# Optimization experiments

Hardware: AMD Instinct MI355X
Metric: run time of the kernel (lower is better)

Reference implementation:

```python
import jax, jax.numpy as jnp
import numpy as np

_BYPASS_THR = 0.99          # assumed v16._BYPASS_THR
_EML_CLAMP = 10000.0        # eml_clamp passed to __init__
COMPLEX = jnp.complex64     # v16.DTYPE


def eml_exact(l, r):
    # EML 'exact' combine: exp(log(l) * log(r)) in the complex domain.
    # This continuous relaxation reproduces mul/pow/add-like behaviour used
    return jnp.exp(jnp.log(l) * jnp.log(r))


def setup_inputs() -> dict:
    key = jax.random.key(0)
    k1, k2, k3, k4 = jax.random.split(key, 4)
    S, depth, B = 16, 5, 131072
    n_leaves = 2 ** depth          # 32
    n_internal = n_leaves - 1      # 31
    x = jax.random.normal(k1, (B,), dtype=jnp.float32)
    y = jax.random.normal(k2, (B,), dtype=jnp.float32)
    # 'uniform' init strategy: leaf ~ N(0,1)*scale, gate ~ N(0,1)*scale + 4
    leaf_logits = jax.random.normal(k3, (S, n_leaves, 3), dtype=jnp.float32)
    blend_logits = jax.random.normal(k4, (S, n_internal, 2), dtype=jnp.float32) + 4.0
    return {"x": x, "y": y, "leaf_logits": leaf_logits, "blend_logits": blend_logits}


def reference(x, y, leaf_logits, blend_logits):
    tau_leaf = 1.0
    tau_gate = 1.0
    C = _EML_CLAMP

    leaf_probs = jax.nn.softmax(leaf_logits / tau_leaf, axis=2)     # (S, L, 3)
    weights = leaf_probs.astype(COMPLEX)

    xc = x.astype(COMPLEX)
    yc = y.astype(COMPLEX)
    ones = jnp.ones_like(xc)
    candidates = jnp.stack([ones, xc, yc], axis=1)                  # (B, 3)

    # current_level: (S, B, n_leaves) complex
    current = jnp.einsum('bc,slc->sbl', candidates, weights)

    gate_levels = []
    eml_outputs = []
    node_idx = 0
    while current.shape[2] > 1:
        n_pairs = current.shape[2] // 2
        left = current[:, :, 0::2]                                  # (S,B,P)
        right = current[:, :, 1::2]
        s = jax.nn.sigmoid(blend_logits[:, node_idx:node_idx + n_pairs] / tau_gate)  # (S,P,2)
        gate_levels.append(s)
        s_left = s[:, :, 0][:, None, :]                             # (S,1,P)
        s_right = s[:, :, 1][:, None, :]
        byp_l = s_left > _BYPASS_THR
        byp_r = s_right > _BYPASS_THR
        oml = 1.0 - s_left
        omr = 1.0 - s_right
        lr = jnp.where(byp_l, 1.0, s_left + oml * left.real)
        li = jnp.where(byp_l, 0.0, oml * left.imag)
        rr = jnp.where(byp_r, 1.0, s_right + omr * right.real)
        ri = jnp.where(byp_r, 0.0, omr * right.imag)
        out = eml_exact(jax.lax.complex(lr, li), jax.lax.complex(rr, ri))
        re = jnp.clip(jnp.nan_to_num(out.real, nan=0.0, posinf=C, neginf=-C), -C, C)
        im = jnp.clip(jnp.nan_to_num(out.imag, nan=0.0, posinf=C, neginf=-C), -C, C)
        current = jax.lax.complex(re, im)
        eml_outputs.append(current)
        node_idx += n_pairs

    gate_probs = jnp.concatenate(gate_levels, axis=1)               # (S, n_internal, 2)
    pred = current[:, :, 0]                                         # (S, B) complex
    return (pred, leaf_probs, gate_probs, *eml_outputs)
```

## Files before the change

### kernel.cpp

```cpp
#include <hip/hip_runtime.h>
#include <math.h>

#define C_CLAMP 10000.0f
#define BYP 0.99f
#define LN2F 0.6931471805599453f

constexpr int NL  = 32;
constexpr int NI  = 31;
constexpr int NG  = 15;
constexpr int BLK = 256;

typedef float f4 __attribute__((ext_vector_type(4)));
typedef float f2 __attribute__((ext_vector_type(2)));

template<bool HASIM>
__device__ __forceinline__ void eml_op(float lre, float lim, float rre, float rim,
                                       float& ore, float& oim) {
    bool ok = fminf(lre, rre) > 0.0f;
    if constexpr (HASIM)
        ok = ok & (fmaxf(fabsf(lim), fabsf(rim)) == 0.0f);

    float t = __log2f(lre) * __log2f(rre);
    float e = __builtin_amdgcn_exp2f(t * LN2F);
    ore = fminf(e, C_CLAMP);
    oim = 0.0f;

    if (__any(!ok)) {
        float a = 0.5f * logf(fmaf(lre, lre, lim * lim));
        float b = atan2f(lim, lre);
        float c = 0.5f * logf(fmaf(rre, rre, rim * rim));
        float d = atan2f(rim, rre);
        float tt = a * c - b * d;
        float th = a * d + b * c;
        float ex = expf(tt);
        float re_ = ex * cosf(th);
        float im_ = ex * sinf(th);
        re_ = __builtin_isnan(re_) ? 0.0f : re_;
        im_ = __builtin_isnan(im_) ? 0.0f : im_;
        re_ = fminf(fmaxf(re_, -C_CLAMP), C_CLAMP);
        im_ = fminf(fmaxf(im_, -C_CLAMP), C_CLAMP);
        if (!ok) { ore = re_; oim = im_; }
    }
}

template<int NP>
__device__ __forceinline__ void do_level(const f4* g4b, int node0,
                                         const float* ire, const float* iim,
                                         float* ore, float* oim) {
#pragma unroll
    for (int p = 0; p < NP; ++p) {
        f4 gg = g4b[node0 - 16 + p];
        float lre = fmaf(gg.y, ire[2 * p],     gg.x);
        float rre = fmaf(gg.w, ire[2 * p + 1], gg.z);
        float lim = gg.y * iim[2 * p];
        float rim = gg.w * iim[2 * p + 1];
        eml_op<true>(lre, lim, rre, rim, ore[p], oim[p]);
    }
}

template<bool PAIRS, int NP>
__device__ __forceinline__ void store_lvl(float* __restrict__ dst, long long sb,
                                          const float* re, const float* im) {
    if constexpr (PAIRS) {
        float* p = dst + sb * (2 * NP);
        if constexpr (NP >= 2) {
#pragma unroll
            for (int q = 0; q < NP; q += 2)
                *reinterpret_cast<f4*>(p + 2 * q) = f4{ re[q], im[q], re[q + 1], im[q + 1] };
        } else {
            *reinterpret_cast<f2*>(p) = f2{ re[0], im[0] };
        }
    } else {
        float* p = dst + sb * NP;
        if constexpr (NP >= 4) {
#pragma unroll
            for (int q = 0; q < NP; q += 4)
                *reinterpret_cast<f4*>(p + q) = f4{ re[q], re[q + 1], re[q + 2], re[q + 3] };
        } else if constexpr (NP == 2) {
            *reinterpret_cast<f2*>(p) = f2{ re[0], re[1] };
        } else {
            p[0] = re[0];
        }
    }
}

template<bool PAIRS>
__global__ __launch_bounds__(BLK, 6) void eml_tree_kernel(
    const float* __restrict__ x, const float* __restrict__ y,
    const float* __restrict__ leaf_logits, const float* __restrict__ blend_logits,
    float* __restrict__ o_pred, float* __restrict__ o_leaf, float* __restrict__ o_gate,
    float* __restrict__ o_l1, float* __restrict__ o_l2, float* __restrict__ o_l3,
    float* __restrict__ o_l4, float* __restrict__ o_l5,
    int B, int blocksPerS)
{
    __shared__ f4    eff4[NL];
    __shared__ f4    g4b[NG];
    __shared__ float graw[NI * 2];
    __shared__ float st1[16][BLK + 1];
    __shared__ float st2[8][BLK + 1];

    const int bid   = blockIdx.x;
    const int s     = bid / blocksPerS;
    const int chunk = bid - s * blocksPerS;
    const int tid   = threadIdx.x;

    if (tid < NL) {
        const float* p = leaf_logits + (s * NL + tid) * 3;
        float a0 = p[0], a1 = p[1], a2 = p[2];
        float m  = fmaxf(a0, fmaxf(a1, a2));
        float e0 = expf(a0 - m), e1 = expf(a1 - m), e2 = expf(a2 - m);
        float inv = 1.0f / (e0 + e1 + e2);
        float w0 = e0 * inv, w1 = e1 * inv, w2 = e2 * inv;

        float sg = 1.0f / (1.0f + expf(-blend_logits[s * NI * 2 + tid]));
        graw[tid] = sg;
        if (sg > BYP) {
            eff4[tid] = f4{ 1.0f, 0.0f, 0.0f, 0.0f };
        } else {
            float om = 1.0f - sg;
            eff4[tid] = f4{ fmaf(om, w0, sg), om * w1, om * w2, 0.0f };
        }
        if (chunk == 0) {
            float* q = o_leaf + s * NL * 3 + tid * 3;
            q[0] = w0; q[1] = w1; q[2] = w2;
        }
    } else if (tid >= 64 && tid < 64 + NG) {
        int i = tid - 64;
        const float* p = blend_logits + s * NI * 2 + (16 + i) * 2;
        float sl = 1.0f / (1.0f + expf(-p[0]));
        float sr = 1.0f / (1.0f + expf(-p[1]));
        graw[(16 + i) * 2]     = sl;
        graw[(16 + i) * 2 + 1] = sr;
        bool bl = sl > BYP, br = sr > BYP;
        g4b[i] = f4{ bl ? 1.0f : sl, bl ? 0.0f : (1.0f - sl),
                     br ? 1.0f : sr, br ? 0.0f : (1.0f - sr) };
    }
    __syncthreads();

    if (chunk == 0 && tid >= 128 && tid < 128 + NI * 2)
        o_gate[s * NI * 2 + (tid - 128)] = graw[tid - 128];

    const int b = chunk * BLK + tid;
    const bool active = b < B;
    const float xv = active ? x[b] : 0.0f;
    const float yv = active ? y[b] : 0.0f;
    const long long sb = (long long)s * B + b;

    if (active) {
        float r2[8], i2[8];
        float b1r[4], b1i[4];
#pragma unroll
        for (int q = 0; q < 8; ++q) {
            const int h0 = (q & 1) * 2;
#pragma unroll
            for (int h = 0; h < 2; ++h) {
                const int p = 2 * q + h;
                f4 ea = eff4[2 * p];
                f4 eb = eff4[2 * p + 1];
                float lre = fmaf(ea.z, yv, fmaf(ea.y, xv, ea.x));
                float rre = fmaf(eb.z, yv, fmaf(eb.y, xv, eb.x));
                eml_op<false>(lre, 0.0f, rre, 0.0f, b1r[h0 + h], b1i[h0 + h]);
                if constexpr (!PAIRS) st1[p][tid] = b1r[h0 + h];
            }
            {
                f4 gg = g4b[q];
                float lre = fmaf(gg.y, b1r[h0],     gg.x);
                float rre = fmaf(gg.w, b1r[h0 + 1], gg.z);
                float lim = gg.y * b1i[h0];
                float rim = gg.w * b1i[h0 + 1];
                eml_op<true>(lre, lim, rre, rim, r2[q], i2[q]);
                if constexpr (!PAIRS) st2[q][tid] = r2[q];
            }
            if (PAIRS && (q & 1)) {
                float* pp = o_l1 + sb * 32 + (q - 1) * 4;
                *reinterpret_cast<f4*>(pp)     = f4{ b1r[0], b1i[0], b1r[1], b1i[1] };
                *reinterpret_cast<f4*>(pp + 4) = f4{ b1r[2], b1i[2], b1r[3], b1i[3] };
            }
        }
        if constexpr (PAIRS) store_lvl<PAIRS, 8>(o_l2, sb, r2, i2);

        float r3[4], i3[4];
        do_level<4>(g4b, 24, r2, i2, r3, i3);
        store_lvl<PAIRS, 4>(o_l3, sb, r3, i3);

        float r4[2], i4[2];
        do_level<2>(g4b, 28, r3, i3, r4, i4);
        store_lvl<PAIRS, 2>(o_l4, sb, r4, i4);

        float r5[1], i5[1];
        do_level<1>(g4b, 30, r4, i4, r5, i5);
        store_lvl<PAIRS, 1>(o_l5, sb, r5, i5);
        store_lvl<PAIRS, 1>(o_pred, sb, r5, i5);
    }

    if constexpr (!PAIRS) {
        __syncthreads();
        const long long b0 = (long long)s * B + (long long)chunk * BLK;
        float* dst1 = o_l1 + b0 * 16;
#pragma unroll
        for (int k = 0; k < 4; ++k) {
            int m  = tid + BLK * k;
            int bl = m >> 2, e0 = (m & 3) << 2;
            if (chunk * BLK + bl < B) {
                f4 v = { st1[e0][bl], st1[e0 + 1][bl], st1[e0 + 2][bl], st1[e0 + 3][bl] };
                *reinterpret_cast<f4*>(dst1 + 4 * (long long)m) = v;
            }
        }
        float* dst2 = o_l2 + b0 * 8;
#pragma unroll
        for (int k = 0; k < 2; ++k) {
            int m  = tid + BLK * k;
            int bl = m >> 1, e0 = (m & 1) << 2;
            if (chunk * BLK + bl < B) {
                f4 v = { st2[e0][bl], st2[e0 + 1][bl], st2[e0 + 2][bl], st2[e0 + 3][bl] };
                *reinterpret_cast<f4*>(dst2 + 4 * (long long)m) = v;
            }
        }
    }
}

extern "C" void kernel_launch(void* const* d_in, const int* in_sizes, int n_in,
                              void* d_out, int out_size, void* d_ws, size_t ws_size,
                              hipStream_t stream) {
    const float* x     = (const float*)d_in[0];
    const float* y     = (const float*)d_in[1];
    const float* leaf  = (const float*)d_in[2];
    const float* blend = (const float*)d_in[3];

    const int B = in_sizes[0];
    const int S = in_sizes[2] / (NL * 3);

    float* out = (float*)d_out;
    const long long SB = (long long)S * B;
    const long long size_pairs = SB * 64 + (long long)S * (NL * 3 + NI * 2);

    const int blocksPerS = (B + BLK - 1) / BLK;
    dim3 grid(S * blocksPerS), block(BLK);

    if ((long long)out_size >= size_pairs) {
        float* o_pred = out;
        float* o_leaf = o_pred + SB * 2;
        float* o_gate = o_leaf + (long long)S * NL * 3;
        float* o_l1   = o_gate + (long long)S * NI * 2;
        float* o_l2   = o_l1 + SB * 32;
        float* o_l3   = o_l2 + SB * 16;
        float* o_l4   = o_l3 + SB * 8;
        float* o_l5   = o_l4 + SB * 4;
        hipLaunchKernelGGL((eml_tree_kernel<true>), grid, block, 0, stream,
                           x, y, leaf, blend,
                           o_pred, o_leaf, o_gate, o_l1, o_l2, o_l3, o_l4, o_l5,
                           B, blocksPerS);
    } else {
        float* o_pred = out;
        float* o_leaf = o_pred + SB;
        float* o_gate = o_leaf + (long long)S * NL * 3;
        float* o_l1   = o_gate + (long long)S * NI * 2;
        float* o_l2   = o_l1 + SB * 16;
        float* o_l3   = o_l2 + SB * 8;
        float* o_l4   = o_l3 + SB * 4;
        float* o_l5   = o_l4 + SB * 2;
        hipLaunchKernelGGL((eml_tree_kernel<false>), grid, block, 0, stream,
                           x, y, leaf, blend,
                           o_pred, o_leaf, o_gate, o_l1, o_l2, o_l3, o_l4, o_l5,
                           B, blocksPerS);
    }
}
```

Baseline: 47.15 us.

## Use persistent-style grid with blocks looping over batch chunks per sample

The grid shrinks from one block per 256-element chunk to about 1024 blocks total, and each block strides over several chunks of the same sample. The per-sample setup (leaf softmax, gate sigmoids into shared memory) is then amortized across many chunks instead of being redone per block. Launch bounds drop from 6 to 4 waves per SIMD, which gives the compiler more registers but lowers occupancy. The non-pairs path adds an extra barrier per iteration to protect the staging buffers.

```diff
diff --git a/kernel.cpp b/kernel.cpp
--- a/kernel.cpp
+++ b/kernel.cpp
@@ -85,13 +85,13 @@
 }
 
 template<bool PAIRS>
-__global__ __launch_bounds__(BLK, 6) void eml_tree_kernel(
+__global__ __launch_bounds__(BLK, 4) void eml_tree_kernel(
     const float* __restrict__ x, const float* __restrict__ y,
     const float* __restrict__ leaf_logits, const float* __restrict__ blend_logits,
     float* __restrict__ o_pred, float* __restrict__ o_leaf, float* __restrict__ o_gate,
     float* __restrict__ o_l1, float* __restrict__ o_l2, float* __restrict__ o_l3,
     float* __restrict__ o_l4, float* __restrict__ o_l5,
-    int B, int blocksPerS)
+    int B, int blocksPerS, int kPerS)
 {
     __shared__ f4    eff4[NL];
     __shared__ f4    g4b[NG];
@@ -99,10 +99,9 @@
     __shared__ float st1[16][BLK + 1];
     __shared__ float st2[8][BLK + 1];
 
-    const int bid   = blockIdx.x;
-    const int s     = bid / blocksPerS;
-    const int chunk = bid - s * blocksPerS;
-    const int tid   = threadIdx.x;
+    const int s   = blockIdx.x / kPerS;
+    const int j   = blockIdx.x - s * kPerS;
+    const int tid = threadIdx.x;
 
     if (tid < NL) {
         const float* p = leaf_logits + (s * NL + tid) * 3;
@@ -120,7 +119,7 @@
             float om = 1.0f - sg;
             eff4[tid] = f4{ fmaf(om, w0, sg), om * w1, om * w2, 0.0f };
         }
-        if (chunk == 0) {
+        if (j == 0) {
             float* q = o_leaf + s * NL * 3 + tid * 3;
             q[0] = w0; q[1] = w1; q[2] = w2;
         }
@@ -137,84 +136,89 @@
     }
     __syncthreads();
 
-    if (chunk == 0 && tid >= 128 && tid < 128 + NI * 2)
+    if (j == 0 && tid >= 128 && tid < 128 + NI * 2)
         o_gate[s * NI * 2 + (tid - 128)] = graw[tid - 128];
 
-    const int b = chunk * BLK + tid;
-    const bool active = b < B;
-    const float xv = active ? x[b] : 0.0f;
-    const float yv = active ? y[b] : 0.0f;
-    const long long sb = (long long)s * B + b;
-
-    if (active) {
-        float r2[8], i2[8];
-        float b1r[4], b1i[4];
-#pragma unroll
-        for (int q = 0; q < 8; ++q) {
-            const int h0 = (q & 1) * 2;
-#pragma unroll
-            for (int h = 0; h < 2; ++h) {
-                const int p = 2 * q + h;
-                f4 ea = eff4[2 * p];
-                f4 eb = eff4[2 * p + 1];
-                float lre = fmaf(ea.z, yv, fmaf(ea.y, xv, ea.x));
-                float rre = fmaf(eb.z, yv, fmaf(eb.y, xv, eb.x));
-                eml_op<false>(lre, 0.0f, rre, 0.0f, b1r[h0 + h], b1i[h0 + h]);
-                if constexpr (!PAIRS) st1[p][tid] = b1r[h0 + h];
+    const long long sBase = (long long)s * B;
+
+    for (int chunk = j; chunk < blocksPerS; chunk += kPerS) {
+        const int b = chunk * BLK + tid;
+        const bool active = b < B;
+        const float xv = active ? x[b] : 0.0f;
+        const float yv = active ? y[b] : 0.0f;
+        const long long sb = sBase + b;
+
+        if (active) {
+            float r2[8], i2[8];
+            float b1r[4], b1i[4];
+#pragma unroll
+            for (int q = 0; q < 8; ++q) {
+                const int h0 = (q & 1) * 2;
+#pragma unroll
+                for (int h = 0; h < 2; ++h) {
+                    const int p = 2 * q + h;
+                    f4 ea = eff4[2 * p];
+                    f4 eb = eff4[2 * p + 1];
+                    float lre = fmaf(ea.z, yv, fmaf(ea.y, xv, ea.x));
+                    float rre = fmaf(eb.z, yv, fmaf(eb.y, xv, eb.x));
+                    eml_op<false>(lre, 0.0f, rre, 0.0f, b1r[h0 + h], b1i[h0 + h]);
+                    if constexpr (!PAIRS) st1[p][tid] = b1r[h0 + h];
+                }
+                {
+                    f4 gg = g4b[q];
+                    float lre = fmaf(gg.y, b1r[h0],     gg.x);
+                    float rre = fmaf(gg.w, b1r[h0 + 1], gg.z);
+                    float lim = gg.y * b1i[h0];
+                    float rim = gg.w * b1i[h0 + 1];
+                    eml_op<true>(lre, lim, rre, rim, r2[q], i2[q]);
+                    if constexpr (!PAIRS) st2[q][tid] = r2[q];
+                }
+                if (PAIRS && (q & 1)) {
+                    float* pp = o_l1 + sb * 32 + (q - 1) * 4;
+                    *reinterpret_cast<f4*>(pp)     = f4{ b1r[0], b1i[0], b1r[1], b1i[1] };
+                    *reinterpret_cast<f4*>(pp + 4) = f4{ b1r[2], b1i[2], b1r[3], b1i[3] };
+                }
             }
-            {
-                f4 gg = g4b[q];
-                float lre = fmaf(gg.y, b1r[h0],     gg.x);
-                float rre = fmaf(gg.w, b1r[h0 + 1], gg.z);
-                float lim = gg.y * b1i[h0];
-                float rim = gg.w * b1i[h0 + 1];
-                eml_op<true>(lre, lim, rre, rim, r2[q], i2[q]);
-                if constexpr (!PAIRS) st2[q][tid] = r2[q];
+            if constexpr (PAIRS) store_lvl<PAIRS, 8>(o_l2, sb, r2, i2);
+
+            float r3[4], i3[4];
+            do_level<4>(g4b, 24, r2, i2, r3, i3);
+            store_lvl<PAIRS, 4>(o_l3, sb, r3, i3);
+
+            float r4[2], i4[2];
+            do_level<2>(g4b, 28, r3, i3, r4, i4);
+            store_lvl<PAIRS, 2>(o_l4, sb, r4, i4);
+
+            float r5[1], i5[1];
+            do_level<1>(g4b, 30, r4, i4, r5, i5);
+            store_lvl<PAIRS, 1>(o_l5, sb, r5, i5);
+            store_lvl<PAIRS, 1>(o_pred, sb, r5, i5);
+        }
+
+        if constexpr (!PAIRS) {
+            __syncthreads();
+            const long long b0 = sBase + (long long)chunk * BLK;
+            float* dst1 = o_l1 + b0 * 16;
+#pragma unroll
+            for (int k = 0; k < 4; ++k) {
+                int m  = tid + BLK * k;
+                int bl = m >> 2, e0 = (m & 3) << 2;
+                if (chunk * BLK + bl < B) {
+                    f4 v = { st1[e0][bl], st1[e0 + 1][bl], st1[e0 + 2][bl], st1[e0 + 3][bl] };
+                    *reinterpret_cast<f4*>(dst1 + 4 * (long long)m) = v;
+                }
             }
-            if (PAIRS && (q & 1)) {
-                float* pp = o_l1 + sb * 32 + (q - 1) * 4;
-                *reinterpret_cast<f4*>(pp)     = f4{ b1r[0], b1i[0], b1r[1], b1i[1] };
-                *reinterpret_cast<f4*>(pp + 4) = f4{ b1r[2], b1i[2], b1r[3], b1i[3] };
+            float* dst2 = o_l2 + b0 * 8;
+#pragma unroll
+            for (int k = 0; k < 2; ++k) {
+                int m  = tid + BLK * k;
+                int bl = m >> 1, e0 = (m & 1) << 2;
+                if (chunk * BLK + bl < B) {
+                    f4 v = { st2[e0][bl], st2[e0 + 1][bl], st2[e0 + 2][bl], st2[e0 + 3][bl] };
+                    *reinterpret_cast<f4*>(dst2 + 4 * (long long)m) = v;
+                }
             }
-        }
-        if constexpr (PAIRS) store_lvl<PAIRS, 8>(o_l2, sb, r2, i2);
-
-        float r3[4], i3[4];
-        do_level<4>(g4b, 24, r2, i2, r3, i3);
-        store_lvl<PAIRS, 4>(o_l3, sb, r3, i3);
-
-        float r4[2], i4[2];
-        do_level<2>(g4b, 28, r3, i3, r4, i4);
-        store_lvl<PAIRS, 2>(o_l4, sb, r4, i4);
-
-        float r5[1], i5[1];
-        do_level<1>(g4b, 30, r4, i4, r5, i5);
-        store_lvl<PAIRS, 1>(o_l5, sb, r5, i5);
-        store_lvl<PAIRS, 1>(o_pred, sb, r5, i5);
-    }
-
-    if constexpr (!PAIRS) {
-        __syncthreads();
-        const long long b0 = (long long)s * B + (long long)chunk * BLK;
-        float* dst1 = o_l1 + b0 * 16;
-#pragma unroll
-        for (int k = 0; k < 4; ++k) {
-            int m  = tid + BLK * k;
-            int bl = m >> 2, e0 = (m & 3) << 2;
-            if (chunk * BLK + bl < B) {
-                f4 v = { st1[e0][bl], st1[e0 + 1][bl], st1[e0 + 2][bl], st1[e0 + 3][bl] };
-                *reinterpret_cast<f4*>(dst1 + 4 * (long long)m) = v;
-            }
-        }
-        float* dst2 = o_l2 + b0 * 8;
-#pragma unroll
-        for (int k = 0; k < 2; ++k) {
-            int m  = tid + BLK * k;
-            int bl = m >> 1, e0 = (m & 1) << 2;
-            if (chunk * BLK + bl < B) {
-                f4 v = { st2[e0][bl], st2[e0 + 1][bl], st2[e0 + 2][bl], st2[e0 + 3][bl] };
-                *reinterpret_cast<f4*>(dst2 + 4 * (long long)m) = v;
-            }
+            __syncthreads();
         }
     }
 }
@@ -235,7 +239,17 @@
     const long long size_pairs = SB * 64 + (long long)S * (NL * 3 + NI * 2);
 
     const int blocksPerS = (B + BLK - 1) / BLK;
-    dim3 grid(S * blocksPerS), block(BLK);
+
+    int target = 1024 / (S > 0 ? S : 1);
+    if (target < 1) target = 1;
+    int kPerS = blocksPerS;
+    if (blocksPerS > target) {
+        kPerS = 1;
+        for (int d = target; d >= 1; --d)
+            if (blocksPerS % d == 0) { kPerS = d; break; }
+    }
+
+    dim3 grid(S * kPerS), block(BLK);
 
     if ((long long)out_size >= size_pairs) {
         float* o_pred = out;
@@ -249,7 +263,7 @@
         hipLaunchKernelGGL((eml_tree_kernel<true>), grid, block, 0, stream,
                            x, y, leaf, blend,
                            o_pred, o_leaf, o_gate, o_l1, o_l2, o_l3, o_l4, o_l5,
-                           B, blocksPerS);
+                           B, blocksPerS, kPerS);
     } else {
         float* o_pred = out;
         float* o_leaf = o_pred + SB;
@@ -262,6 +276,6 @@
         hipLaunchKernelGGL((eml_tree_kernel<false>), grid, block, 0, stream,
                            x, y, leaf, blend,
                            o_pred, o_leaf, o_gate, o_l1, o_l2, o_l3, o_l4, o_l5,
-                           B, blocksPerS);
-    }
-}
+                           B, blocksPerS, kPerS);
+    }
+}
```

After: 55.21 us. 1.17x slower.
